# Kernel optimization log

Measured on AMD Instinct MI355X. Metric: run time of the kernel, lower is better.

The kernel has to match this reference:

```python
import jax, jax.numpy as jnp
import numpy as np

N_NODES = 50000
N_EDGES = 800000
F_DIM = 64
NEG_SLOPE_ATT = 0.2   # GATConv attention LeakyReLU
NEG_SLOPE_ACT = 0.01  # nn.LeakyReLU default between layers


def setup_inputs() -> dict:
    key = jax.random.key(0)
    ks = jax.random.split(key, 10)
    s = 1.0 / np.sqrt(F_DIM)
    return {
        "x": jax.random.normal(ks[0], (N_NODES, F_DIM), jnp.float32),
        "edge_index": jax.random.randint(ks[1], (2, N_EDGES), 0, N_NODES, jnp.int64),
        "W0": jax.random.normal(ks[2], (F_DIM, F_DIM), jnp.float32) * s,
        "a_src0": jax.random.normal(ks[3], (F_DIM,), jnp.float32) * s,
        "a_dst0": jax.random.normal(ks[4], (F_DIM,), jnp.float32) * s,
        "b0": jnp.zeros((F_DIM,), jnp.float32),
        "W1": jax.random.normal(ks[5], (F_DIM, F_DIM), jnp.float32) * s,
        "a_src1": jax.random.normal(ks[6], (F_DIM,), jnp.float32) * s,
        "a_dst1": jax.random.normal(ks[7], (F_DIM,), jnp.float32) * s,
        "b1": jnp.zeros((F_DIM,), jnp.float32),
    }


def _gat_layer(x, src, dst, W, a_src, a_dst, b, n_nodes):
    # x: [N,F]; src/dst: [E'] (self-loops included)
    h = x @ W                                   # [N,F]
    alpha_s = h @ a_src                          # [N]
    alpha_d = h @ a_dst                          # [N]
    e = jax.nn.leaky_relu(alpha_s[src] + alpha_d[dst], NEG_SLOPE_ATT)  # [E']
    # scatter-softmax over incoming edges per destination node
    m = jax.ops.segment_max(e, dst, num_segments=n_nodes)              # [N]
    ex = jnp.exp(e - m[dst])                                           # [E']
    z = jax.ops.segment_sum(ex, dst, num_segments=n_nodes)             # [N]
    alpha = ex / (z[dst] + 1e-16)                                      # [E']
    out = jax.ops.segment_sum(h[src] * alpha[:, None], dst, num_segments=n_nodes)
    return out + b


def reference(x, edge_index, W0, a_src0, a_dst0, b0, W1, a_src1, a_dst1, b1):
    n = x.shape[0]
    loops = jnp.arange(n, dtype=edge_index.dtype)
    src = jnp.concatenate([edge_index[0], loops])  # add_self_loops=True
    dst = jnp.concatenate([edge_index[1], loops])
    h = _gat_layer(x, src, dst, W0, a_src0, a_dst0, b0, n)
    h = jax.nn.leaky_relu(h, NEG_SLOPE_ACT)
    h = _gat_layer(h, src, dst, W1, a_src1, a_dst1, b1, n)
    h = jax.nn.leaky_relu(h, NEG_SLOPE_ACT)
    return h + x  # residual with original input features
```

## Files before the change

### kernel.cpp

```cpp
#include <hip/hip_runtime.h>
#include <math.h>

#define NNODES 50000
#define NEDGES 800000
#define ETOT   850000
#define F      64
#define NB     782
#define CAP    1408
#define LIN_BLOCKS 3125
#define AGG_BLOCKS 12500
#define SBLK   256
#define SIT    13
#define SEPB   (256 * SIT)

typedef unsigned short u16;
typedef unsigned int   u32;

__device__ __forceinline__ u32 f2bf2(float a, float b) {
    u32 ua = __float_as_uint(a), ub = __float_as_uint(b);
    ua = (ua + 0x7FFFu + ((ua >> 16) & 1u)) >> 16;
    ub = (ub + 0x7FFFu + ((ub >> 16) & 1u)) >> 16;
    return ua | (ub << 16);
}

struct LinSmem {
    float Ws[F * F];
    float xs[16][F + 1];
    float asv[F], adv[F];
};

__device__ __forceinline__ void linear_body(
    LinSmem& sm,
    const float* __restrict__ x, const float* __restrict__ W,
    const float* __restrict__ a_src, const float* __restrict__ a_dst,
    u16* __restrict__ h16, float* __restrict__ as_, float* __restrict__ ad_,
    int blk)
{
    const int tid = threadIdx.x;
    const int wv  = tid >> 6;
    const int ln  = tid & 63;
    const int q   = ln >> 4;
    const int fl4 = (ln & 15) * 4;
    const int nb  = wv * 4 + q;
    const int node = blk * 16 + nb;

    for (int i = tid * 4; i < F * F; i += 1024)
        *(float4*)&sm.Ws[i] = *(const float4*)&W[i];
    if (tid < F) { sm.asv[tid] = a_src[tid]; sm.adv[tid] = a_dst[tid]; }
    {
        const int n  = tid >> 4;
        const int c4 = (tid & 15) * 4;
        const float4 v = *(const float4*)&x[(size_t)(blk * 16 + n) * F + c4];
        sm.xs[n][c4] = v.x; sm.xs[n][c4+1] = v.y;
        sm.xs[n][c4+2] = v.z; sm.xs[n][c4+3] = v.w;
    }
    __syncthreads();

    float4 acc = {0.f, 0.f, 0.f, 0.f};
#pragma unroll
    for (int k = 0; k < F; ++k) {
        const float xv = sm.xs[nb][k];
        const float4 w = *(const float4*)&sm.Ws[k * F + fl4];
        acc.x = fmaf(xv, w.x, acc.x);
        acc.y = fmaf(xv, w.y, acc.y);
        acc.z = fmaf(xv, w.z, acc.z);
        acc.w = fmaf(xv, w.w, acc.w);
    }

    uint2 p;
    p.x = f2bf2(acc.x, acc.y);
    p.y = f2bf2(acc.z, acc.w);
    *(uint2*)(h16 + (size_t)node * F + fl4) = p;

    float vs = acc.x * sm.asv[fl4] + acc.y * sm.asv[fl4+1]
             + acc.z * sm.asv[fl4+2] + acc.w * sm.asv[fl4+3];
    float vd = acc.x * sm.adv[fl4] + acc.y * sm.adv[fl4+1]
             + acc.z * sm.adv[fl4+2] + acc.w * sm.adv[fl4+3];
#pragma unroll
    for (int off = 1; off < 16; off <<= 1) {
        vs += __shfl_xor(vs, off, 64);
        vd += __shfl_xor(vd, off, 64);
    }
    if ((ln & 15) == 0) { as_[node] = vs; ad_[node] = vd; }
}

__global__ __launch_bounds__(256) void stage_linear1(
    const float* __restrict__ x, const float* __restrict__ W,
    const float* __restrict__ a_src, const float* __restrict__ a_dst,
    u16* __restrict__ h16, float* __restrict__ as_, float* __restrict__ ad_,
    const int* __restrict__ src, const int* __restrict__ dst,
    int* __restrict__ gcur, u32* __restrict__ stg)
{
    __shared__ LinSmem sm;
    if (blockIdx.x < SBLK) {
        int* cnt  = (int*)&sm;
        int* lcur = cnt + NB;
        for (int i = threadIdx.x; i < NB; i += 256) cnt[i] = 0;
        __syncthreads();
        const int base = blockIdx.x * SEPB;
#pragma unroll
        for (int it = 0; it < SIT; ++it) {
            const int e = base + it * 256 + threadIdx.x;
            if (e < ETOT) {
                const int d = (e < NEDGES) ? dst[e] : (e - NEDGES);
                atomicAdd(&cnt[d >> 6], 1);
            }
        }
        __syncthreads();
        for (int i = threadIdx.x; i < NB; i += 256)
            lcur[i] = cnt[i] ? (i * CAP + atomicAdd(&gcur[i], cnt[i])) : 0;
        __syncthreads();
#pragma unroll
        for (int it = 0; it < SIT; ++it) {
            const int e = base + it * 256 + threadIdx.x;
            if (e < ETOT) {
                int s, d;
                if (e < NEDGES) { s = src[e]; d = dst[e]; }
                else            { s = e - NEDGES; d = s; }
                const int p = atomicAdd(&lcur[d >> 6], 1);
                stg[p] = ((u32)(d & 63) << 16) | (u32)s;
            }
        }
        return;
    }
    linear_body(sm, x, W, a_src, a_dst, h16, as_, ad_, blockIdx.x - SBLK);
}

__global__ __launch_bounds__(256) void bucket_csr(
    const int* __restrict__ gcur, const u32* __restrict__ stg,
    u16* __restrict__ csr, int* __restrict__ rowptr, int* __restrict__ rowcnt)
{
    __shared__ int cnt[64];
    const int b = blockIdx.x;
    const int nbase = b << 6;
    const int nr  = (NNODES - nbase < 64) ? (NNODES - nbase) : 64;
    const int beg = b * CAP;
    const int m   = gcur[b];

    if (threadIdx.x < 64) cnt[threadIdx.x] = 0;
    __syncthreads();
    for (int i = threadIdx.x; i < m; i += 256)
        atomicAdd(&cnt[stg[beg + i] >> 16], 1);
    __syncthreads();
    if (threadIdx.x < 64) {
        const int v = cnt[threadIdx.x];
        int incl = v;
#pragma unroll
        for (int off = 1; off < 64; off <<= 1) {
            const int t = __shfl_up(incl, off, 64);
            if (threadIdx.x >= off) incl += t;
        }
        const int pos = beg + incl - v;
        cnt[threadIdx.x] = pos;
        if (threadIdx.x < nr) {
            rowptr[nbase + threadIdx.x] = pos;
            rowcnt[nbase + threadIdx.x] = v;
        }
    }
    __syncthreads();
    for (int i = threadIdx.x; i < m; i += 256) {
        const u32 pk = stg[beg + i];
        const int pos = atomicAdd(&cnt[pk >> 16], 1);
        csr[pos] = (u16)(pk & 0xFFFFu);
    }
}

template<int MODE>
__global__ __launch_bounds__(256) void gat_agg(
    const int* __restrict__ rowptr, const int* __restrict__ rowcnt,
    const u16* __restrict__ csr, const u16* __restrict__ hin,
    const float* __restrict__ as_, const float* __restrict__ ad_,
    const float* __restrict__ bias,
    const float* __restrict__ Wn, const float* __restrict__ an_s,
    const float* __restrict__ an_d,
    u16* __restrict__ hout, float* __restrict__ as_out, float* __restrict__ ad_out,
    const float* __restrict__ resid, float* __restrict__ out)
{
    __shared__ float Ws[MODE == 0 ? F * F : 1];
    __shared__ float asv[MODE == 0 ? F : 1], adv[MODE == 0 ? F : 1];
    __shared__ float xrow[MODE == 0 ? 4 : 1][F];

    const int tid  = threadIdx.x;
    const int wv   = tid >> 6;
    const int ln   = tid & 63;
    const int node = blockIdx.x * 4 + wv;
    const int g    = ln >> 3;
    const int l    = ln & 7;

    if constexpr (MODE == 0) {
        for (int i = tid * 4; i < F * F; i += 1024)
            *(float4*)&Ws[i] = *(const float4*)&Wn[i];
        if (tid < F) { asv[tid] = an_s[tid]; adv[tid] = an_d[tid]; }
        __syncthreads();
    }

    const float ad_n = ad_[node];
    const int beg = rowptr[node];
    const int end = beg + rowcnt[node];

    float a0=0.f,a1=0.f,a2=0.f,a3=0.f,a4=0.f,a5=0.f,a6=0.f,a7=0.f;
    float z = 0.f;
    int i = beg + g;
    for (; i + 8 < end; i += 16) {
        const int s1 = csr[i];
        const int s2 = csr[i + 8];
        const float as1v = as_[s1];
        const float as2v = as_[s2];
        const uint4 h1 = ((const uint4*)(hin + (size_t)s1 * F))[l];
        const uint4 h2 = ((const uint4*)(hin + (size_t)s2 * F))[l];
        float t1 = as1v + ad_n; t1 = (t1 > 0.f) ? t1 : 0.2f * t1;
        float t2 = as2v + ad_n; t2 = (t2 > 0.f) ? t2 : 0.2f * t2;
        const float e1 = __expf(t1);
        const float e2 = __expf(t2);
        z += e1 + e2;
        a0 = fmaf(e1, __uint_as_float(h1.x << 16),         a0);
        a1 = fmaf(e1, __uint_as_float(h1.x & 0xFFFF0000u), a1);
        a2 = fmaf(e1, __uint_as_float(h1.y << 16),         a2);
        a3 = fmaf(e1, __uint_as_float(h1.y & 0xFFFF0000u), a3);
        a4 = fmaf(e1, __uint_as_float(h1.z << 16),         a4);
        a5 = fmaf(e1, __uint_as_float(h1.z & 0xFFFF0000u), a5);
        a6 = fmaf(e1, __uint_as_float(h1.w << 16),         a6);
        a7 = fmaf(e1, __uint_as_float(h1.w & 0xFFFF0000u), a7);
        a0 = fmaf(e2, __uint_as_float(h2.x << 16),         a0);
        a1 = fmaf(e2, __uint_as_float(h2.x & 0xFFFF0000u), a1);
        a2 = fmaf(e2, __uint_as_float(h2.y << 16),         a2);
        a3 = fmaf(e2, __uint_as_float(h2.y & 0xFFFF0000u), a3);
        a4 = fmaf(e2, __uint_as_float(h2.z << 16),         a4);
        a5 = fmaf(e2, __uint_as_float(h2.z & 0xFFFF0000u), a5);
        a6 = fmaf(e2, __uint_as_float(h2.w << 16),         a6);
        a7 = fmaf(e2, __uint_as_float(h2.w & 0xFFFF0000u), a7);
    }
    if (i < end) {
        const int s1 = csr[i];
        float t1 = as_[s1] + ad_n; t1 = (t1 > 0.f) ? t1 : 0.2f * t1;
        const float e1 = __expf(t1);
        const uint4 h1 = ((const uint4*)(hin + (size_t)s1 * F))[l];
        z += e1;
        a0 = fmaf(e1, __uint_as_float(h1.x << 16),         a0);
        a1 = fmaf(e1, __uint_as_float(h1.x & 0xFFFF0000u), a1);
        a2 = fmaf(e1, __uint_as_float(h1.y << 16),         a2);
        a3 = fmaf(e1, __uint_as_float(h1.y & 0xFFFF0000u), a3);
        a4 = fmaf(e1, __uint_as_float(h1.z << 16),         a4);
        a5 = fmaf(e1, __uint_as_float(h1.z & 0xFFFF0000u), a5);
        a6 = fmaf(e1, __uint_as_float(h1.w << 16),         a6);
        a7 = fmaf(e1, __uint_as_float(h1.w & 0xFFFF0000u), a7);
    }
#pragma unroll
    for (int off = 8; off < 64; off <<= 1) {
        a0 += __shfl_xor(a0, off, 64); a1 += __shfl_xor(a1, off, 64);
        a2 += __shfl_xor(a2, off, 64); a3 += __shfl_xor(a3, off, 64);
        a4 += __shfl_xor(a4, off, 64); a5 += __shfl_xor(a5, off, 64);
        a6 += __shfl_xor(a6, off, 64); a7 += __shfl_xor(a7, off, 64);
        z  += __shfl_xor(z,  off, 64);
    }

    const float inv = 1.f / (z + 1e-16f);
    const float4 b0v = *(const float4*)&bias[l * 8];
    const float4 b1v = *(const float4*)&bias[l * 8 + 4];
    float v0 = a0 * inv + b0v.x, v1 = a1 * inv + b0v.y;
    float v2 = a2 * inv + b0v.z, v3 = a3 * inv + b0v.w;
    float v4 = a4 * inv + b1v.x, v5 = a5 * inv + b1v.y;
    float v6 = a6 * inv + b1v.z, v7 = a7 * inv + b1v.w;
    v0 = (v0 > 0.f) ? v0 : 0.01f * v0;  v1 = (v1 > 0.f) ? v1 : 0.01f * v1;
    v2 = (v2 > 0.f) ? v2 : 0.01f * v2;  v3 = (v3 > 0.f) ? v3 : 0.01f * v3;
    v4 = (v4 > 0.f) ? v4 : 0.01f * v4;  v5 = (v5 > 0.f) ? v5 : 0.01f * v5;
    v6 = (v6 > 0.f) ? v6 : 0.01f * v6;  v7 = (v7 > 0.f) ? v7 : 0.01f * v7;

    if constexpr (MODE == 0) {
        if (g == 0) {
            float4 w0; w0.x = v0; w0.y = v1; w0.z = v2; w0.w = v3;
            float4 w1; w1.x = v4; w1.y = v5; w1.z = v6; w1.w = v7;
            *(float4*)&xrow[wv][l * 8]     = w0;
            *(float4*)&xrow[wv][l * 8 + 4] = w1;
        }
        __syncthreads();

        const int q  = ln >> 4;
        const int c4 = (ln & 15) * 4;
        float4 o = {0.f, 0.f, 0.f, 0.f};
#pragma unroll
        for (int kk = 0; kk < 16; ++kk) {
            const int k = q * 16 + kk;
            const float xv = xrow[wv][k];
            const float4 w = *(const float4*)&Ws[k * F + c4];
            o.x = fmaf(xv, w.x, o.x);
            o.y = fmaf(xv, w.y, o.y);
            o.z = fmaf(xv, w.z, o.z);
            o.w = fmaf(xv, w.w, o.w);
        }
        o.x += __shfl_xor(o.x, 16, 64); o.x += __shfl_xor(o.x, 32, 64);
        o.y += __shfl_xor(o.y, 16, 64); o.y += __shfl_xor(o.y, 32, 64);
        o.z += __shfl_xor(o.z, 16, 64); o.z += __shfl_xor(o.z, 32, 64);
        o.w += __shfl_xor(o.w, 16, 64); o.w += __shfl_xor(o.w, 32, 64);

        float vs = o.x * asv[c4] + o.y * asv[c4+1] + o.z * asv[c4+2] + o.w * asv[c4+3];
        float vd = o.x * adv[c4] + o.y * adv[c4+1] + o.z * adv[c4+2] + o.w * adv[c4+3];
#pragma unroll
        for (int off = 1; off < 16; off <<= 1) {
            vs += __shfl_xor(vs, off, 64);
            vd += __shfl_xor(vd, off, 64);
        }
        if (ln == 0) { as_out[node] = vs; ad_out[node] = vd; }
        if (q == 0) {
            uint2 p;
            p.x = f2bf2(o.x, o.y);
            p.y = f2bf2(o.z, o.w);
            *(uint2*)&hout[(size_t)node * F + c4] = p;
        }
    } else {
        if (g == 0) {
            const float4 r0 = *(const float4*)(resid + (size_t)node * F + l * 8);
            const float4 r1 = *(const float4*)(resid + (size_t)node * F + l * 8 + 4);
            float4 o0, o1;
            o0.x = v0 + r0.x; o0.y = v1 + r0.y; o0.z = v2 + r0.z; o0.w = v3 + r0.w;
            o1.x = v4 + r1.x; o1.y = v5 + r1.y; o1.z = v6 + r1.z; o1.w = v7 + r1.w;
            *(float4*)(out + (size_t)node * F + l * 8)     = o0;
            *(float4*)(out + (size_t)node * F + l * 8 + 4) = o1;
        }
    }
}

extern "C" void kernel_launch(void* const* d_in, const int* in_sizes, int n_in,
                              void* d_out, int out_size, void* d_ws, size_t ws_size,
                              hipStream_t stream)
{
    const float* x   = (const float*)d_in[0];
    const int*   ei  = (const int*)  d_in[1];
    const float* W0  = (const float*)d_in[2];
    const float* as0 = (const float*)d_in[3];
    const float* ad0 = (const float*)d_in[4];
    const float* b0  = (const float*)d_in[5];
    const float* W1  = (const float*)d_in[6];
    const float* as1 = (const float*)d_in[7];
    const float* ad1 = (const float*)d_in[8];
    const float* b1  = (const float*)d_in[9];
    float* out = (float*)d_out;

    const int* src = ei;
    const int* dst = ei + NEDGES;

    char* ws = (char*)d_ws;
    u16*   h16    = (u16*)ws;   ws += (size_t)NNODES * F * 2;
    u16*   h2_16  = (u16*)ws;   ws += (size_t)NNODES * F * 2;
    float* as_    = (float*)ws; ws += (size_t)NNODES * 4;
    float* ad_    = (float*)ws; ws += (size_t)NNODES * 4;
    float* as2    = (float*)ws; ws += (size_t)NNODES * 4;
    float* ad2    = (float*)ws; ws += (size_t)NNODES * 4;
    int*   rowptr = (int*)ws;   ws += (size_t)NNODES * 4;
    int*   rowcnt = (int*)ws;   ws += (size_t)NNODES * 4;
    int*   gcur   = (int*)ws;   ws += (size_t)NB * 4;
    u32*   stg    = (u32*)ws;   ws += (size_t)NB * CAP * 4;
    u16*   csr    = (u16*)ws;   ws += (size_t)NB * CAP * 2;

    hipMemsetAsync(gcur, 0, (size_t)NB * 4, stream);
    stage_linear1<<<SBLK + LIN_BLOCKS, 256, 0, stream>>>(
        x, W0, as0, ad0, h16, as_, ad_, src, dst, gcur, stg);
    bucket_csr<<<NB, 256, 0, stream>>>(gcur, stg, csr, rowptr, rowcnt);

    gat_agg<0><<<AGG_BLOCKS, 256, 0, stream>>>(
        rowptr, rowcnt, csr, h16, as_, ad_, b0,
        W1, as1, ad1, h2_16, as2, ad2, nullptr, nullptr);
    gat_agg<1><<<AGG_BLOCKS, 256, 0, stream>>>(
        rowptr, rowcnt, csr, h2_16, as2, ad2, b1,
        nullptr, nullptr, nullptr, nullptr, nullptr, nullptr, x, out);
}
```

Baseline: 192.8 us.

## Map eight-lane groups to nodes in GAT aggregation and batch the fused linear

The aggregation kernel now gives each 8-lane group its own destination node, so a block covers 32 nodes instead of one wave per node. Each group walks that node's edges sequentially, which removes the cross-group shuffle reductions. The fused next-layer linear transform now runs as a batched 32x64 by 64x64 product from a padded shared tile, so W is loaded once per 32 nodes rather than per 4. The trade-off is less memory-level parallelism per node and load imbalance inside a wave when degrees differ, since lanes idle until the longest neighbor list is done.

Result: faster. 171.7 us (-10.9%).

```diff
diff --git a/kernel.cpp b/kernel.cpp
--- a/kernel.cpp
+++ b/kernel.cpp
@@ -8,7 +8,7 @@
 #define NB     782
 #define CAP    1408
 #define LIN_BLOCKS 3125
-#define AGG_BLOCKS 12500
+#define AGG_BLOCKS 1563
 #define SBLK   256
 #define SIT    13
 #define SEPB   (256 * SIT)
@@ -165,6 +165,7 @@
     }
 }
 
+#define XSP 68
 template<int MODE>
 __global__ __launch_bounds__(256) void gat_agg(
     const int* __restrict__ rowptr, const int* __restrict__ rowcnt,
@@ -178,38 +179,42 @@
 {
     __shared__ float Ws[MODE == 0 ? F * F : 1];
     __shared__ float asv[MODE == 0 ? F : 1], adv[MODE == 0 ? F : 1];
-    __shared__ float xrow[MODE == 0 ? 4 : 1][F];
-
-    const int tid  = threadIdx.x;
-    const int wv   = tid >> 6;
-    const int ln   = tid & 63;
-    const int node = blockIdx.x * 4 + wv;
-    const int g    = ln >> 3;
-    const int l    = ln & 7;
+    __shared__ float xs[MODE == 0 ? 32 * XSP : 1];
+
+    const int tid = threadIdx.x;
+    const int ln  = tid & 63;
+    const int g   = ln >> 3;
+    const int l   = ln & 7;
+    const int nb  = (tid >> 6) * 8 + g;
+    const int node = blockIdx.x * 32 + nb;
+    const bool valid = node < NNODES;
 
     if constexpr (MODE == 0) {
         for (int i = tid * 4; i < F * F; i += 1024)
             *(float4*)&Ws[i] = *(const float4*)&Wn[i];
         if (tid < F) { asv[tid] = an_s[tid]; adv[tid] = an_d[tid]; }
-        __syncthreads();
-    }
-
-    const float ad_n = ad_[node];
-    const int beg = rowptr[node];
-    const int end = beg + rowcnt[node];
+    }
+
+    int beg = 0, cnt = 0;
+    float ad_n = 0.f;
+    if (valid) {
+        beg  = rowptr[node];
+        cnt  = rowcnt[node];
+        ad_n = ad_[node];
+    }
 
     float a0=0.f,a1=0.f,a2=0.f,a3=0.f,a4=0.f,a5=0.f,a6=0.f,a7=0.f;
     float z = 0.f;
-    int i = beg + g;
-    for (; i + 8 < end; i += 16) {
-        const int s1 = csr[i];
-        const int s2 = csr[i + 8];
-        const float as1v = as_[s1];
-        const float as2v = as_[s2];
+    int i = 0;
+    for (; i + 1 < cnt; i += 2) {
+        const int s1 = csr[beg + i];
+        const int s2 = csr[beg + i + 1];
+        const float r1 = as_[s1] + ad_n;
+        const float r2 = as_[s2] + ad_n;
         const uint4 h1 = ((const uint4*)(hin + (size_t)s1 * F))[l];
         const uint4 h2 = ((const uint4*)(hin + (size_t)s2 * F))[l];
-        float t1 = as1v + ad_n; t1 = (t1 > 0.f) ? t1 : 0.2f * t1;
-        float t2 = as2v + ad_n; t2 = (t2 > 0.f) ? t2 : 0.2f * t2;
+        const float t1 = (r1 > 0.f) ? r1 : 0.2f * r1;
+        const float t2 = (r2 > 0.f) ? r2 : 0.2f * r2;
         const float e1 = __expf(t1);
         const float e2 = __expf(t2);
         z += e1 + e2;
@@ -230,11 +235,12 @@
         a6 = fmaf(e2, __uint_as_float(h2.w << 16),         a6);
         a7 = fmaf(e2, __uint_as_float(h2.w & 0xFFFF0000u), a7);
     }
-    if (i < end) {
-        const int s1 = csr[i];
-        float t1 = as_[s1] + ad_n; t1 = (t1 > 0.f) ? t1 : 0.2f * t1;
+    if (i < cnt) {
+        const int s1 = csr[beg + i];
+        const float r1 = as_[s1] + ad_n;
+        const uint4 h1 = ((const uint4*)(hin + (size_t)s1 * F))[l];
+        const float t1 = (r1 > 0.f) ? r1 : 0.2f * r1;
         const float e1 = __expf(t1);
-        const uint4 h1 = ((const uint4*)(hin + (size_t)s1 * F))[l];
         z += e1;
         a0 = fmaf(e1, __uint_as_float(h1.x << 16),         a0);
         a1 = fmaf(e1, __uint_as_float(h1.x & 0xFFFF0000u), a1);
@@ -244,14 +250,6 @@
         a5 = fmaf(e1, __uint_as_float(h1.z & 0xFFFF0000u), a5);
         a6 = fmaf(e1, __uint_as_float(h1.w << 16),         a6);
         a7 = fmaf(e1, __uint_as_float(h1.w & 0xFFFF0000u), a7);
-    }
-#pragma unroll
-    for (int off = 8; off < 64; off <<= 1) {
-        a0 += __shfl_xor(a0, off, 64); a1 += __shfl_xor(a1, off, 64);
-        a2 += __shfl_xor(a2, off, 64); a3 += __shfl_xor(a3, off, 64);
-        a4 += __shfl_xor(a4, off, 64); a5 += __shfl_xor(a5, off, 64);
-        a6 += __shfl_xor(a6, off, 64); a7 += __shfl_xor(a7, off, 64);
-        z  += __shfl_xor(z,  off, 64);
     }
 
     const float inv = 1.f / (z + 1e-16f);
@@ -267,48 +265,44 @@
     v6 = (v6 > 0.f) ? v6 : 0.01f * v6;  v7 = (v7 > 0.f) ? v7 : 0.01f * v7;
 
     if constexpr (MODE == 0) {
-        if (g == 0) {
+        {
             float4 w0; w0.x = v0; w0.y = v1; w0.z = v2; w0.w = v3;
             float4 w1; w1.x = v4; w1.y = v5; w1.z = v6; w1.w = v7;
-            *(float4*)&xrow[wv][l * 8]     = w0;
-            *(float4*)&xrow[wv][l * 8 + 4] = w1;
+            const int xb = nb * XSP + l * 8;
+            *(float4*)&xs[xb]     = w0;
+            *(float4*)&xs[xb + 4] = w1;
         }
         __syncthreads();
 
-        const int q  = ln >> 4;
-        const int c4 = (ln & 15) * 4;
-        float4 o = {0.f, 0.f, 0.f, 0.f};
-#pragma unroll
-        for (int kk = 0; kk < 16; ++kk) {
-            const int k = q * 16 + kk;
-            const float xv = xrow[wv][k];
-            const float4 w = *(const float4*)&Ws[k * F + c4];
-            o.x = fmaf(xv, w.x, o.x);
-            o.y = fmaf(xv, w.y, o.y);
-            o.z = fmaf(xv, w.z, o.z);
-            o.w = fmaf(xv, w.w, o.w);
-        }
-        o.x += __shfl_xor(o.x, 16, 64); o.x += __shfl_xor(o.x, 32, 64);
-        o.y += __shfl_xor(o.y, 16, 64); o.y += __shfl_xor(o.y, 32, 64);
-        o.z += __shfl_xor(o.z, 16, 64); o.z += __shfl_xor(o.z, 32, 64);
-        o.w += __shfl_xor(o.w, 16, 64); o.w += __shfl_xor(o.w, 32, 64);
-
-        float vs = o.x * asv[c4] + o.y * asv[c4+1] + o.z * asv[c4+2] + o.w * asv[c4+3];
-        float vd = o.x * adv[c4] + o.y * adv[c4+1] + o.z * adv[c4+2] + o.w * adv[c4+3];
-#pragma unroll
-        for (int off = 1; off < 16; off <<= 1) {
-            vs += __shfl_xor(vs, off, 64);
-            vd += __shfl_xor(vd, off, 64);
-        }
-        if (ln == 0) { as_out[node] = vs; ad_out[node] = vd; }
-        if (q == 0) {
-            uint2 p;
-            p.x = f2bf2(o.x, o.y);
-            p.y = f2bf2(o.z, o.w);
-            *(uint2*)&hout[(size_t)node * F + c4] = p;
+        const int nb2 = tid >> 3;
+        const int c0  = (tid & 7) * 8;
+        float o0=0.f,o1=0.f,o2=0.f,o3=0.f,o4=0.f,o5=0.f,o6=0.f,o7=0.f;
+#pragma unroll 8
+        for (int k = 0; k < F; ++k) {
+            const float xv = xs[nb2 * XSP + k];
+            const float4 wa = *(const float4*)&Ws[k * F + c0];
+            const float4 wb = *(const float4*)&Ws[k * F + c0 + 4];
+            o0 = fmaf(xv, wa.x, o0); o1 = fmaf(xv, wa.y, o1);
+            o2 = fmaf(xv, wa.z, o2); o3 = fmaf(xv, wa.w, o3);
+            o4 = fmaf(xv, wb.x, o4); o5 = fmaf(xv, wb.y, o5);
+            o6 = fmaf(xv, wb.z, o6); o7 = fmaf(xv, wb.w, o7);
+        }
+        const int node2 = blockIdx.x * 32 + nb2;
+        float vs = o0*asv[c0]   + o1*asv[c0+1] + o2*asv[c0+2] + o3*asv[c0+3]
+                 + o4*asv[c0+4] + o5*asv[c0+5] + o6*asv[c0+6] + o7*asv[c0+7];
+        float vd = o0*adv[c0]   + o1*adv[c0+1] + o2*adv[c0+2] + o3*adv[c0+3]
+                 + o4*adv[c0+4] + o5*adv[c0+5] + o6*adv[c0+6] + o7*adv[c0+7];
+        vs += __shfl_xor(vs, 1, 64); vs += __shfl_xor(vs, 2, 64); vs += __shfl_xor(vs, 4, 64);
+        vd += __shfl_xor(vd, 1, 64); vd += __shfl_xor(vd, 2, 64); vd += __shfl_xor(vd, 4, 64);
+        if (node2 < NNODES) {
+            if ((tid & 7) == 0) { as_out[node2] = vs; ad_out[node2] = vd; }
+            uint4 p;
+            p.x = f2bf2(o0, o1); p.y = f2bf2(o2, o3);
+            p.z = f2bf2(o4, o5); p.w = f2bf2(o6, o7);
+            *(uint4*)&hout[(size_t)node2 * F + c0] = p;
         }
     } else {
-        if (g == 0) {
+        if (valid) {
             const float4 r0 = *(const float4*)(resid + (size_t)node * F + l * 8);
             const float4 r1 = *(const float4*)(resid + (size_t)node * F + l * 8 + 4);
             float4 o0, o1;
```
